# Optimization experiments

Measured on AMD Instinct MI355X. Metric: run time of the kernel, lower is better.

Reference implementation:

```python
import jax, jax.numpy as jnp
import numpy as np

EMBED_DIM = 1024
HEADS = 16
HEAD_DIM = EMBED_DIM // HEADS


def setup_inputs() -> dict:
    key = jax.random.key(0)
    ks = jax.random.split(key, 9)
    D = EMBED_DIM
    s = 1.0 / np.sqrt(D)
    x = jax.random.normal(ks[0], (4, 2048, D), dtype=jnp.float32)
    Wq = jax.random.uniform(ks[1], (D, D), jnp.float32, -s, s)
    bq = jnp.zeros((D,), jnp.float32)
    Wk = jax.random.uniform(ks[2], (D, D), jnp.float32, -s, s)
    bk = jnp.zeros((D,), jnp.float32)
    Wv = jax.random.uniform(ks[3], (D, D), jnp.float32, -s, s)
    bv = jnp.zeros((D,), jnp.float32)
    Wo = jax.random.uniform(ks[4], (D, D), jnp.float32, -s, s)
    bo = jnp.zeros((D,), jnp.float32)
    gamma = jnp.ones((D,), jnp.float32)
    beta = jnp.zeros((D,), jnp.float32)
    return {"x": x, "Wq": Wq, "bq": bq, "Wk": Wk, "bk": bk,
            "Wv": Wv, "bv": bv, "Wo": Wo, "bo": bo,
            "gamma": gamma, "beta": beta}


def reference(x, Wq, bq, Wk, bk, Wv, bv, Wo, bo, gamma, beta):
    B, S, D = x.shape
    H, Dh = HEADS, HEAD_DIM
    # projections -> [B, H, S, Dh]
    q = (x @ Wq + bq).reshape(B, S, H, Dh).transpose(0, 2, 1, 3)
    k = (x @ Wk + bk).reshape(B, S, H, Dh).transpose(0, 2, 1, 3)
    v = (x @ Wv + bv).reshape(B, S, H, Dh).transpose(0, 2, 1, 3)
    scores = jnp.einsum('bhqd,bhkd->bhqk', q, k) / jnp.sqrt(jnp.float32(Dh))
    attn = jax.nn.softmax(scores, axis=-1)  # dropout is identity in eval
    ctx = jnp.einsum('bhqk,bhkd->bhqd', attn, v)
    ctx = ctx.transpose(0, 2, 1, 3).reshape(B, S, D)
    out = ctx @ Wo + bo
    # residual + LayerNorm (eps=1e-5, torch default)
    h = out + x
    mu = jnp.mean(h, axis=-1, keepdims=True)
    var = jnp.mean(jnp.square(h - mu), axis=-1, keepdims=True)
    return (h - mu) * jax.lax.rsqrt(var + 1e-5) * gamma + beta
```

## Files before the change

kernel.cpp:

```cpp
#include <hip/hip_runtime.h>
#include <hip/hip_bf16.h>
#include <stdint.h>

typedef short sh4 __attribute__((ext_vector_type(4)));
typedef short sh8 __attribute__((ext_vector_type(8)));
typedef float fl4 __attribute__((ext_vector_type(4)));
typedef float f32x4 __attribute__((ext_vector_type(4)));
typedef float f32x16 __attribute__((ext_vector_type(16)));
typedef uint32_t u32x4 __attribute__((ext_vector_type(4)));

static __device__ __forceinline__ short f2bf(float f) {
  union { float f; uint32_t u; } v;
  v.f = f;
  uint32_t r = v.u + 0x7fffu + ((v.u >> 16) & 1u);
  return (short)(r >> 16);
}

static __device__ __forceinline__ uint32_t cvt_pk_bf16(float a, float b) {
  uint32_t r;
  asm("v_cvt_pk_bf16_f32 %0, %1, %2" : "=v"(r) : "v"(a), "v"(b));
  return r;
}

static __device__ __forceinline__ void pl32swap(uint32_t& a, uint32_t& b) {
  asm volatile("v_permlane32_swap_b32 %0, %1" : "+v"(a), "+v"(b));
}

static __device__ __forceinline__ void gload_lds16(const void* g, void* l) {
  __builtin_amdgcn_global_load_lds((const __attribute__((address_space(1))) void*)g,
                                   (__attribute__((address_space(3))) void*)l, 16, 0, 0);
}

__global__ __launch_bounds__(256) void k_wt(const float* __restrict__ Wq, const float* __restrict__ Wk,
                                            const float* __restrict__ Wv, const float* __restrict__ Wo,
                                            short* __restrict__ Tq, short* __restrict__ Tk,
                                            short* __restrict__ Tv, short* __restrict__ To) {
  const float* W = blockIdx.z == 0 ? Wq : blockIdx.z == 1 ? Wk : blockIdx.z == 2 ? Wv : Wo;
  short* T = blockIdx.z == 0 ? Tq : blockIdx.z == 1 ? Tk : blockIdx.z == 2 ? Tv : To;
  __shared__ float tile[32][33];
  int n0 = blockIdx.x * 32, k0 = blockIdx.y * 32;
  int tx = threadIdx.x, ty = threadIdx.y;
#pragma unroll
  for (int p = 0; p < 4; p++) tile[ty + 8 * p][tx] = W[(size_t)(k0 + ty + 8 * p) * 1024 + n0 + tx];
  __syncthreads();
#pragma unroll
  for (int p = 0; p < 4; p++) T[(size_t)(n0 + ty + 8 * p) * 1024 + k0 + tx] = f2bf(tile[tx][ty + 8 * p]);
}

__global__ __launch_bounds__(256) void k_cvtx(const float* __restrict__ x, short* __restrict__ o) {
  int i = blockIdx.x * 256 + threadIdx.x;
  fl4 v = ((const fl4*)x)[i];
  sh4 r;
#pragma unroll
  for (int j = 0; j < 4; j++) r[j] = f2bf(v[j]);
  ((sh4*)o)[i] = r;
}

#define GEMM_PIPE_LOOP(STAGE_BODY, COMPUTE_BODY)                         \
  STAGE_BODY(0, 0);                                                      \
  STAGE_BODY(1, 1);                                                      \
  {                                                                      \
    int bufc = 0, bufs = 2;                                              \
    for (int it = 0; it < 32; it++) {                                    \
      if (it < 31)                                                       \
        asm volatile("s_waitcnt vmcnt(4)" ::: "memory");                 \
      else                                                               \
        asm volatile("s_waitcnt vmcnt(0)" ::: "memory");                 \
      __builtin_amdgcn_s_barrier();                                      \
      if (it + 2 < 32) { STAGE_BODY(it + 2, bufs); }                     \
      __builtin_amdgcn_sched_barrier(0);                                 \
      { int buf = bufc; COMPUTE_BODY }                                   \
      bufc = bufc == 2 ? 0 : bufc + 1;                                   \
      bufs = bufs == 2 ? 0 : bufs + 1;                                   \
      asm volatile("" ::: "memory");                                     \
    }                                                                    \
  }

__global__ __launch_bounds__(256) void k_qk(const short* __restrict__ A, const short* __restrict__ WT2,
                                            const float* __restrict__ bq, const float* __restrict__ bk,
                                            short* __restrict__ Qo, short* __restrict__ Ko, float qscale) {
  __shared__ __align__(16) short As[3][128 * 32];
  __shared__ __align__(16) short Bs[3][128 * 32];
  const int xcd = blockIdx.x & 7, j = blockIdx.x >> 3;
  const int m0 = (xcd + 8 * (j & 7)) * 128, n0 = (j >> 3) * 128;
  const int sec = n0 >> 10;
  const float* bias = sec == 0 ? bq : bk;
  short* Out = sec == 0 ? Qo : Ko;
  const float scale = sec == 0 ? qscale : 1.f;
  const int t = threadIdx.x;
  const int lane = t & 63, w = t >> 6;
  const int wr = w >> 1, wc = w & 1;
  const int l15 = lane & 15, g = lane >> 4;
  f32x4 acc[4][4];
#pragma unroll
  for (int mi = 0; mi < 4; mi++)
#pragma unroll
    for (int ni = 0; ni < 4; ni++) acc[mi][ni] = (f32x4){0.f, 0.f, 0.f, 0.f};

#define QK_STAGE(kt, buf)                                                                     \
  {                                                                                           \
    int r0 = w * 32;                                                                          \
    _Pragma("unroll") for (int i = 0; i < 2; i++) {                                           \
      int row = r0 + i * 16 + (lane >> 2);                                                    \
      gload_lds16(&A[(size_t)(m0 + row) * 1024 + (kt) * 32 + (lane & 3) * 8],                 \
                  &As[buf][(r0 + i * 16) * 32]);                                              \
      gload_lds16(&WT2[(size_t)(n0 + row) * 1024 + (kt) * 32 + (lane & 3) * 8],               \
                  &Bs[buf][(r0 + i * 16) * 32]);                                              \
    }                                                                                         \
  }

#define QK_COMPUTE                                                                            \
  sh8 a[4], b[4];                                                                             \
  _Pragma("unroll") for (int i = 0; i < 4; i++)                                               \
      a[i] = *(sh8*)&As[buf][(wr * 64 + i * 16 + l15) * 32 + g * 8];                          \
  _Pragma("unroll") for (int i = 0; i < 4; i++)                                               \
      b[i] = *(sh8*)&Bs[buf][(wc * 64 + i * 16 + l15) * 32 + g * 8];                          \
  _Pragma("unroll") for (int mi = 0; mi < 4; mi++)                                            \
      _Pragma("unroll") for (int ni = 0; ni < 4; ni++)                                        \
          acc[mi][ni] = __builtin_amdgcn_mfma_f32_16x16x32_bf16(b[ni], a[mi], acc[mi][ni], 0, 0, 0);

  GEMM_PIPE_LOOP(QK_STAGE, QK_COMPUTE)

#pragma unroll
  for (int ni = 0; ni < 4; ni++) {
    int nbase = n0 + wc * 64 + ni * 16 + g * 4;
    int nn0 = nbase & 1023;
    fl4 bv4 = *(const fl4*)&bias[nn0];
    int h = nn0 >> 6, dh0 = nn0 & 63;
#pragma unroll
    for (int mi = 0; mi < 4; mi++) {
      int m = m0 + wr * 64 + mi * 16 + l15;
      int bb = m >> 11, s = m & 2047;
      uint2 dd;
      dd.x = cvt_pk_bf16((acc[mi][ni][0] + bv4[0]) * scale, (acc[mi][ni][1] + bv4[1]) * scale);
      dd.y = cvt_pk_bf16((acc[mi][ni][2] + bv4[2]) * scale, (acc[mi][ni][3] + bv4[3]) * scale);
      *(uint2*)&Out[(((size_t)bb * 16 + h) * 2048 + s) * 64 + dh0] = dd;
    }
  }
}

__global__ __launch_bounds__(256) void k_v(const short* __restrict__ A, const short* __restrict__ WTv,
                                           const float* __restrict__ bv, short* __restrict__ Vo) {
  __shared__ __align__(16) short As[3][128 * 32];
  __shared__ __align__(16) short Bs[3][128 * 32];
  const int xcd = blockIdx.x & 7, j = blockIdx.x >> 3;
  const int m0 = (xcd + 8 * (j & 7)) * 128, n0 = (j >> 3) * 128;
  const int t = threadIdx.x;
  const int lane = t & 63, w = t >> 6;
  const int wr = w >> 1, wc = w & 1;
  const int l15 = lane & 15, g = lane >> 4;
  f32x4 acc[4][4];
#pragma unroll
  for (int mi = 0; mi < 4; mi++)
#pragma unroll
    for (int ni = 0; ni < 4; ni++) acc[mi][ni] = (f32x4){0.f, 0.f, 0.f, 0.f};

#define V_STAGE(kt, buf)                                                                      \
  {                                                                                           \
    int r0 = w * 32;                                                                          \
    _Pragma("unroll") for (int i = 0; i < 2; i++) {                                           \
      int row = r0 + i * 16 + (lane >> 2);                                                    \
      gload_lds16(&A[(size_t)(m0 + row) * 1024 + (kt) * 32 + (lane & 3) * 8],                 \
                  &As[buf][(r0 + i * 16) * 32]);                                              \
      gload_lds16(&WTv[(size_t)(n0 + row) * 1024 + (kt) * 32 + (lane & 3) * 8],               \
                  &Bs[buf][(r0 + i * 16) * 32]);                                              \
    }                                                                                         \
  }

#define V_COMPUTE                                                                             \
  sh8 a[4], b[4];                                                                             \
  _Pragma("unroll") for (int i = 0; i < 4; i++)                                               \
      a[i] = *(sh8*)&As[buf][(wr * 64 + i * 16 + l15) * 32 + g * 8];                          \
  _Pragma("unroll") for (int i = 0; i < 4; i++)                                               \
      b[i] = *(sh8*)&Bs[buf][(wc * 64 + i * 16 + l15) * 32 + g * 8];                          \
  _Pragma("unroll") for (int mi = 0; mi < 4; mi++)                                            \
      _Pragma("unroll") for (int ni = 0; ni < 4; ni++)                                        \
          acc[mi][ni] = __builtin_amdgcn_mfma_f32_16x16x32_bf16(a[mi], b[ni], acc[mi][ni], 0, 0, 0);

  GEMM_PIPE_LOOP(V_STAGE, V_COMPUTE)

#pragma unroll
  for (int ni = 0; ni < 4; ni++) {
    int col = n0 + wc * 64 + ni * 16 + l15;
    int nn = col & 1023;
    float bvv = bv[nn];
    int h = nn >> 6, dh = nn & 63;
#pragma unroll
    for (int mi = 0; mi < 4; mi++) {
      int mr = m0 + wr * 64 + mi * 16 + g * 4;
      int bb = mr >> 11, s = mr & 2047;
      uint2 dd;
      dd.x = cvt_pk_bf16(acc[mi][ni][0] + bvv, acc[mi][ni][1] + bvv);
      dd.y = cvt_pk_bf16(acc[mi][ni][2] + bvv, acc[mi][ni][3] + bvv);
      *(uint2*)&Vo[(((size_t)bb * 16 + h) * 64 + dh) * 2048 + s] = dd;
    }
  }
}

__global__ __launch_bounds__(256) void k_oproj(const short* __restrict__ A, const short* __restrict__ BT,
                                               const float* __restrict__ bias, const float* __restrict__ X,
                                               float* __restrict__ Out) {
  __shared__ __align__(16) short As[3][128 * 32];
  __shared__ __align__(16) short Bs[3][128 * 32];
  const int xcd = blockIdx.x & 7, j = blockIdx.x >> 3;
  const int m0 = (xcd + 8 * (j & 7)) * 128, n0 = (j >> 3) * 128;
  const int t = threadIdx.x;
  const int lane = t & 63, w = t >> 6;
  const int wr = w >> 1, wc = w & 1;
  const int l15 = lane & 15, g = lane >> 4;
  f32x4 acc[4][4];
#pragma unroll
  for (int mi = 0; mi < 4; mi++)
#pragma unroll
    for (int ni = 0; ni < 4; ni++) acc[mi][ni] = (f32x4){0.f, 0.f, 0.f, 0.f};

#define O_STAGE(kt, buf)                                                                      \
  {                                                                                           \
    int r0 = w * 32;                                                                          \
    _Pragma("unroll") for (int i = 0; i < 2; i++) {                                           \
      int row = r0 + i * 16 + (lane >> 2);                                                    \
      gload_lds16(&A[(size_t)(m0 + row) * 1024 + (kt) * 32 + (lane & 3) * 8],                 \
                  &As[buf][(r0 + i * 16) * 32]);                                              \
      gload_lds16(&BT[(size_t)(n0 + row) * 1024 + (kt) * 32 + (lane & 3) * 8],                \
                  &Bs[buf][(r0 + i * 16) * 32]);                                              \
    }                                                                                         \
  }

#define O_COMPUTE                                                                             \
  sh8 a[4], b[4];                                                                             \
  _Pragma("unroll") for (int i = 0; i < 4; i++)                                               \
      a[i] = *(sh8*)&As[buf][(wr * 64 + i * 16 + l15) * 32 + g * 8];                          \
  _Pragma("unroll") for (int i = 0; i < 4; i++)                                               \
      b[i] = *(sh8*)&Bs[buf][(wc * 64 + i * 16 + l15) * 32 + g * 8];                          \
  _Pragma("unroll") for (int mi = 0; mi < 4; mi++)                                            \
      _Pragma("unroll") for (int ni = 0; ni < 4; ni++)                                        \
          acc[mi][ni] = __builtin_amdgcn_mfma_f32_16x16x32_bf16(b[ni], a[mi], acc[mi][ni], 0, 0, 0);

  GEMM_PIPE_LOOP(O_STAGE, O_COMPUTE)

#pragma unroll
  for (int ni = 0; ni < 4; ni++) {
    int nbase = n0 + wc * 64 + ni * 16 + g * 4;
    fl4 bv4 = *(const fl4*)&bias[nbase];
#pragma unroll
    for (int mi = 0; mi < 4; mi++) {
      int m = m0 + wr * 64 + mi * 16 + l15;
      fl4 xv = *(const fl4*)&X[(size_t)m * 1024 + nbase];
      fl4 r;
#pragma unroll
      for (int e = 0; e < 4; e++) r[e] = acc[mi][ni][e] + bv4[e] + xv[e];
      *(fl4*)&Out[(size_t)m * 1024 + nbase] = r;
    }
  }
}

__global__ __launch_bounds__(512, 4) void k_attn(const short* __restrict__ Q, const short* __restrict__ K,
                                                 const short* __restrict__ Vt, short* __restrict__ CTX) {
  const int nid = (blockIdx.x & 7) * 64 + (blockIdx.x >> 3);
  const int qbi = nid & 7, h = (nid >> 3) & 15, b = nid >> 7;
  const int q0 = qbi * 256;
  const size_t ho = (((size_t)b * 16 + h) * 2048) * 64;
  const short* Qh = Q + ho;
  const short* Kh = K + ho;
  const short* Vh = Vt + ho;
  __shared__ __align__(16) short Ks[3][8 * 512];
  __shared__ __align__(16) short Vs[3][8 * 512];
  const int t = threadIdx.x, lane = t & 63, w = t >> 6;
  const int l31 = lane & 31, hi = lane >> 5;

  sh8 qreg[4];
#pragma unroll
  for (int ks = 0; ks < 4; ks++)
    qreg[ks] = *(const sh8*)&Qh[(size_t)(q0 + w * 32 + l31) * 64 + ks * 16 + hi * 8];

  f32x16 oc0, oc1;
#pragma unroll
  for (int r = 0; r < 16; r++) { oc0[r] = 0.f; oc1[r] = 0.f; }
  float l_s = 0.f;

  auto stage = [&](int kt, int buf) {
    gload_lds16(&Kh[(size_t)(kt * 64 + (w >> 2) * 32 + l31) * 64 + (w & 3) * 16 + hi * 8],
                (char*)&Ks[buf][0] + w * 1024);
    gload_lds16(&Vh[(size_t)((w >> 2) * 32 + l31) * 2048 + kt * 64 + (w & 3) * 16 + hi * 8],
                (char*)&Vs[buf][0] + w * 1024);
  };

  stage(0, 0);
  stage(1, 1);
  int bufc = 0, bufs = 2;

  for (int kt = 0; kt < 32; kt++) {
    if (kt < 31)
      asm volatile("s_waitcnt vmcnt(2)" ::: "memory");
    else
      asm volatile("s_waitcnt vmcnt(0)" ::: "memory");
    __builtin_amdgcn_s_barrier();
    if (kt + 2 < 32) stage(kt + 2, bufs);
    __builtin_amdgcn_sched_barrier(0);

    f32x16 s0, s1;
#pragma unroll
    for (int r = 0; r < 16; r++) { s0[r] = 0.f; s1[r] = 0.f; }
    __builtin_amdgcn_s_setprio(1);
#pragma unroll
    for (int ks = 0; ks < 4; ks++) {
      sh8 ak0 = *(sh8*)((char*)&Ks[bufc][0] + ks * 1024 + lane * 16);
      sh8 ak1 = *(sh8*)((char*)&Ks[bufc][0] + (4 + ks) * 1024 + lane * 16);
      s0 = __builtin_amdgcn_mfma_f32_32x32x16_bf16(ak0, qreg[ks], s0, 0, 0, 0);
      s1 = __builtin_amdgcn_mfma_f32_32x32x16_bf16(ak1, qreg[ks], s1, 0, 0, 0);
    }
    __builtin_amdgcn_s_setprio(0);

    float ps = 0.f;
#pragma unroll
    for (int r = 0; r < 16; r++) { s0[r] = __builtin_amdgcn_exp2f(s0[r]); ps += s0[r]; }
#pragma unroll
    for (int r = 0; r < 16; r++) { s1[r] = __builtin_amdgcn_exp2f(s1[r]); ps += s1[r]; }
    l_s += ps;

    u32x4 pw0, pw1, pw2, pw3;
    {
      uint32_t a0 = cvt_pk_bf16(s0[0], s0[1]), a1 = cvt_pk_bf16(s0[2], s0[3]);
      uint32_t b0 = cvt_pk_bf16(s0[4], s0[5]), b1 = cvt_pk_bf16(s0[6], s0[7]);
      uint32_t c0 = cvt_pk_bf16(s0[8], s0[9]), c1 = cvt_pk_bf16(s0[10], s0[11]);
      uint32_t d0 = cvt_pk_bf16(s0[12], s0[13]), d1 = cvt_pk_bf16(s0[14], s0[15]);
      pl32swap(a0, b0); pl32swap(a1, b1); pl32swap(c0, d0); pl32swap(c1, d1);
      pw0 = (u32x4){a0, a1, b0, b1};
      pw1 = (u32x4){c0, c1, d0, d1};
      a0 = cvt_pk_bf16(s1[0], s1[1]); a1 = cvt_pk_bf16(s1[2], s1[3]);
      b0 = cvt_pk_bf16(s1[4], s1[5]); b1 = cvt_pk_bf16(s1[6], s1[7]);
      c0 = cvt_pk_bf16(s1[8], s1[9]); c1 = cvt_pk_bf16(s1[10], s1[11]);
      d0 = cvt_pk_bf16(s1[12], s1[13]); d1 = cvt_pk_bf16(s1[14], s1[15]);
      pl32swap(a0, b0); pl32swap(a1, b1); pl32swap(c0, d0); pl32swap(c1, d1);
      pw2 = (u32x4){a0, a1, b0, b1};
      pw3 = (u32x4){c0, c1, d0, d1};
    }
    sh8 pb0 = __builtin_bit_cast(sh8, pw0), pb1 = __builtin_bit_cast(sh8, pw1);
    sh8 pb2 = __builtin_bit_cast(sh8, pw2), pb3 = __builtin_bit_cast(sh8, pw3);

    __builtin_amdgcn_s_setprio(1);
#pragma unroll
    for (int ks = 0; ks < 4; ks++) {
      sh8 pb = ks == 0 ? pb0 : ks == 1 ? pb1 : ks == 2 ? pb2 : pb3;
      sh8 av0 = *(sh8*)((char*)&Vs[bufc][0] + ks * 1024 + lane * 16);
      sh8 av1 = *(sh8*)((char*)&Vs[bufc][0] + (4 + ks) * 1024 + lane * 16);
      oc0 = __builtin_amdgcn_mfma_f32_32x32x16_bf16(av0, pb, oc0, 0, 0, 0);
      oc1 = __builtin_amdgcn_mfma_f32_32x32x16_bf16(av1, pb, oc1, 0, 0, 0);
    }
    __builtin_amdgcn_s_setprio(0);
    bufc = bufc == 2 ? 0 : bufc + 1;
    bufs = bufs == 2 ? 0 : bufs + 1;
    asm volatile("" ::: "memory");
  }

  l_s += __shfl_xor(l_s, 32);
  float li = 1.f / l_s;
  int s = q0 + w * 32 + l31;
  size_t obase = (((size_t)b * 2048 + s) * 16 + h) * 64;
#pragma unroll
  for (int rq = 0; rq < 4; rq++) {
    uint2 dd;
    dd.x = cvt_pk_bf16(oc0[4 * rq] * li, oc0[4 * rq + 1] * li);
    dd.y = cvt_pk_bf16(oc0[4 * rq + 2] * li, oc0[4 * rq + 3] * li);
    *(uint2*)&CTX[obase + rq * 8 + hi * 4] = dd;
    dd.x = cvt_pk_bf16(oc1[4 * rq] * li, oc1[4 * rq + 1] * li);
    dd.y = cvt_pk_bf16(oc1[4 * rq + 2] * li, oc1[4 * rq + 3] * li);
    *(uint2*)&CTX[obase + 32 + rq * 8 + hi * 4] = dd;
  }
}

__global__ __launch_bounds__(256) void k_ln(float* __restrict__ Out, const float* __restrict__ gamma,
                                            const float* __restrict__ beta) {
  int row = blockIdx.x * 4 + (threadIdx.x >> 6);
  int lane = threadIdx.x & 63;
  float* p = Out + (size_t)row * 1024;
  fl4 v[4];
  float s = 0.f, s2 = 0.f;
#pragma unroll
  for (int j = 0; j < 4; j++) {
    v[j] = *(fl4*)&p[lane * 4 + j * 256];
#pragma unroll
    for (int e = 0; e < 4; e++) { s += v[j][e]; s2 += v[j][e] * v[j][e]; }
  }
#pragma unroll
  for (int off = 1; off < 64; off <<= 1) {
    s += __shfl_xor(s, off);
    s2 += __shfl_xor(s2, off);
  }
  float mu = s * (1.f / 1024.f);
  float var = s2 * (1.f / 1024.f) - mu * mu;
  float inv = rsqrtf(var + 1e-5f);
#pragma unroll
  for (int j = 0; j < 4; j++) {
    fl4 r;
#pragma unroll
    for (int e = 0; e < 4; e++) {
      int c = lane * 4 + j * 256 + e;
      r[e] = (v[j][e] - mu) * inv * gamma[c] + beta[c];
    }
    *(fl4*)&p[lane * 4 + j * 256] = r;
  }
}

extern "C" void kernel_launch(void* const* d_in, const int* in_sizes, int n_in,
                              void* d_out, int out_size, void* d_ws, size_t ws_size,
                              hipStream_t stream) {
  (void)in_sizes; (void)n_in; (void)out_size; (void)ws_size;
  const float* x = (const float*)d_in[0];
  const float* Wq = (const float*)d_in[1];
  const float* bq = (const float*)d_in[2];
  const float* Wk = (const float*)d_in[3];
  const float* bk = (const float*)d_in[4];
  const float* Wv = (const float*)d_in[5];
  const float* bv = (const float*)d_in[6];
  const float* Wo = (const float*)d_in[7];
  const float* bo = (const float*)d_in[8];
  const float* gamma = (const float*)d_in[9];
  const float* beta = (const float*)d_in[10];
  float* out = (float*)d_out;
  char* ws = (char*)d_ws;
  short* xbf = (short*)(ws);
  short* wtq = (short*)(ws + (16ull << 20));
  short* wtk = (short*)(ws + (18ull << 20));
  short* wtv = (short*)(ws + (20ull << 20));
  short* wto = (short*)(ws + (22ull << 20));
  short* qb  = (short*)(ws + (24ull << 20));
  short* kbuf = (short*)(ws + (40ull << 20));
  short* vbuf = (short*)(ws + (56ull << 20));
  short* ctx = (short*)(ws + (72ull << 20));

  const float QSCALE = 0.125f * 1.44269504088896f;

  k_wt<<<dim3(32, 32, 4), dim3(32, 8), 0, stream>>>(Wq, Wk, Wv, Wo, wtq, wtk, wtv, wto);
  k_cvtx<<<8192, 256, 0, stream>>>(x, xbf);
  k_qk<<<1024, 256, 0, stream>>>(xbf, wtq, bq, bk, qb, kbuf, QSCALE);
  k_v<<<512, 256, 0, stream>>>(xbf, wtv, bv, vbuf);
  k_attn<<<512, 512, 0, stream>>>(qb, kbuf, vbuf, ctx);
  k_oproj<<<512, 256, 0, stream>>>(ctx, wto, bo, x, out);
  k_ln<<<2048, 256, 0, stream>>>(out, gamma, beta);
}
```

Baseline: 213.9 us.

## Software-pipeline attention loop: overlap PV of previous tile with QK of current

Restructures the attention inner loop so the P·V MFMAs for tile kt-1 are issued right after the Q·K MFMAs for tile kt, letting exp/convert work overlap with matrix ops. The packed probabilities are carried across iterations in registers and a drain step follows the loop. V gets a fourth LDS buffer so the previous tile's V stays valid while the next ones are prefetched. This costs extra LDS and more live registers, which could lower occupancy under the launch bounds.

```diff
diff --git a/kernel.cpp b/kernel.cpp
--- a/kernel.cpp
+++ b/kernel.cpp
@@ -264,7 +264,7 @@
   const short* Kh = K + ho;
   const short* Vh = Vt + ho;
   __shared__ __align__(16) short Ks[3][8 * 512];
-  __shared__ __align__(16) short Vs[3][8 * 512];
+  __shared__ __align__(16) short Vs[4][8 * 512];
   const int t = threadIdx.x, lane = t & 63, w = t >> 6;
   const int l31 = lane & 31, hi = lane >> 5;
 
@@ -273,21 +273,25 @@
   for (int ks = 0; ks < 4; ks++)
     qreg[ks] = *(const sh8*)&Qh[(size_t)(q0 + w * 32 + l31) * 64 + ks * 16 + hi * 8];
 
-  f32x16 oc0, oc1;
-#pragma unroll
-  for (int r = 0; r < 16; r++) { oc0[r] = 0.f; oc1[r] = 0.f; }
+  f32x16 zinit;
+#pragma unroll
+  for (int r = 0; r < 16; r++) zinit[r] = 0.f;
+
+  f32x16 oc0 = zinit, oc1 = zinit;
   float l_s = 0.f;
-
-  auto stage = [&](int kt, int buf) {
+  u32x4 pwp[4];
+
+  auto stageK = [&](int kt, int buf) {
     gload_lds16(&Kh[(size_t)(kt * 64 + (w >> 2) * 32 + l31) * 64 + (w & 3) * 16 + hi * 8],
                 (char*)&Ks[buf][0] + w * 1024);
+  };
+  auto stageV = [&](int kt, int buf) {
     gload_lds16(&Vh[(size_t)((w >> 2) * 32 + l31) * 2048 + kt * 64 + (w & 3) * 16 + hi * 8],
                 (char*)&Vs[buf][0] + w * 1024);
   };
 
-  stage(0, 0);
-  stage(1, 1);
-  int bufc = 0, bufs = 2;
+  stageK(0, 0); stageV(0, 0);
+  stageK(1, 1); stageV(1, 1);
 
   for (int kt = 0; kt < 32; kt++) {
     if (kt < 31)
@@ -295,19 +299,35 @@
     else
       asm volatile("s_waitcnt vmcnt(0)" ::: "memory");
     __builtin_amdgcn_s_barrier();
-    if (kt + 2 < 32) stage(kt + 2, bufs);
+    if (kt + 2 < 32) { stageK(kt + 2, (kt + 2) % 3); stageV(kt + 2, (kt + 2) & 3); }
     __builtin_amdgcn_sched_barrier(0);
+    const int kbuf = kt % 3;
 
     f32x16 s0, s1;
-#pragma unroll
-    for (int r = 0; r < 16; r++) { s0[r] = 0.f; s1[r] = 0.f; }
     __builtin_amdgcn_s_setprio(1);
 #pragma unroll
     for (int ks = 0; ks < 4; ks++) {
-      sh8 ak0 = *(sh8*)((char*)&Ks[bufc][0] + ks * 1024 + lane * 16);
-      sh8 ak1 = *(sh8*)((char*)&Ks[bufc][0] + (4 + ks) * 1024 + lane * 16);
-      s0 = __builtin_amdgcn_mfma_f32_32x32x16_bf16(ak0, qreg[ks], s0, 0, 0, 0);
-      s1 = __builtin_amdgcn_mfma_f32_32x32x16_bf16(ak1, qreg[ks], s1, 0, 0, 0);
+      sh8 ak0 = *(sh8*)((char*)&Ks[kbuf][0] + ks * 1024 + lane * 16);
+      sh8 ak1 = *(sh8*)((char*)&Ks[kbuf][0] + (4 + ks) * 1024 + lane * 16);
+      if (ks == 0) {
+        s0 = __builtin_amdgcn_mfma_f32_32x32x16_bf16(ak0, qreg[0], zinit, 0, 0, 0);
+        s1 = __builtin_amdgcn_mfma_f32_32x32x16_bf16(ak1, qreg[0], zinit, 0, 0, 0);
+      } else {
+        s0 = __builtin_amdgcn_mfma_f32_32x32x16_bf16(ak0, qreg[ks], s0, 0, 0, 0);
+        s1 = __builtin_amdgcn_mfma_f32_32x32x16_bf16(ak1, qreg[ks], s1, 0, 0, 0);
+      }
+    }
+
+    if (kt > 0) {
+      const int vb = (kt - 1) & 3;
+#pragma unroll
+      for (int ks = 0; ks < 4; ks++) {
+        sh8 pb = __builtin_bit_cast(sh8, pwp[ks]);
+        sh8 av0 = *(sh8*)((char*)&Vs[vb][0] + ks * 1024 + lane * 16);
+        sh8 av1 = *(sh8*)((char*)&Vs[vb][0] + (4 + ks) * 1024 + lane * 16);
+        oc0 = __builtin_amdgcn_mfma_f32_32x32x16_bf16(av0, pb, oc0, 0, 0, 0);
+        oc1 = __builtin_amdgcn_mfma_f32_32x32x16_bf16(av1, pb, oc1, 0, 0, 0);
+      }
     }
     __builtin_amdgcn_s_setprio(0);
 
@@ -318,39 +338,37 @@
     for (int r = 0; r < 16; r++) { s1[r] = __builtin_amdgcn_exp2f(s1[r]); ps += s1[r]; }
     l_s += ps;
 
-    u32x4 pw0, pw1, pw2, pw3;
     {
       uint32_t a0 = cvt_pk_bf16(s0[0], s0[1]), a1 = cvt_pk_bf16(s0[2], s0[3]);
       uint32_t b0 = cvt_pk_bf16(s0[4], s0[5]), b1 = cvt_pk_bf16(s0[6], s0[7]);
       uint32_t c0 = cvt_pk_bf16(s0[8], s0[9]), c1 = cvt_pk_bf16(s0[10], s0[11]);
       uint32_t d0 = cvt_pk_bf16(s0[12], s0[13]), d1 = cvt_pk_bf16(s0[14], s0[15]);
       pl32swap(a0, b0); pl32swap(a1, b1); pl32swap(c0, d0); pl32swap(c1, d1);
-      pw0 = (u32x4){a0, a1, b0, b1};
-      pw1 = (u32x4){c0, c1, d0, d1};
+      pwp[0] = (u32x4){a0, a1, b0, b1};
+      pwp[1] = (u32x4){c0, c1, d0, d1};
       a0 = cvt_pk_bf16(s1[0], s1[1]); a1 = cvt_pk_bf16(s1[2], s1[3]);
       b0 = cvt_pk_bf16(s1[4], s1[5]); b1 = cvt_pk_bf16(s1[6], s1[7]);
       c0 = cvt_pk_bf16(s1[8], s1[9]); c1 = cvt_pk_bf16(s1[10], s1[11]);
       d0 = cvt_pk_bf16(s1[12], s1[13]); d1 = cvt_pk_bf16(s1[14], s1[15]);
       pl32swap(a0, b0); pl32swap(a1, b1); pl32swap(c0, d0); pl32swap(c1, d1);
-      pw2 = (u32x4){a0, a1, b0, b1};
-      pw3 = (u32x4){c0, c1, d0, d1};
-    }
-    sh8 pb0 = __builtin_bit_cast(sh8, pw0), pb1 = __builtin_bit_cast(sh8, pw1);
-    sh8 pb2 = __builtin_bit_cast(sh8, pw2), pb3 = __builtin_bit_cast(sh8, pw3);
-
+      pwp[2] = (u32x4){a0, a1, b0, b1};
+      pwp[3] = (u32x4){c0, c1, d0, d1};
+    }
+    asm volatile("" ::: "memory");
+  }
+
+  {
+    const int vb = 31 & 3;
     __builtin_amdgcn_s_setprio(1);
 #pragma unroll
     for (int ks = 0; ks < 4; ks++) {
-      sh8 pb = ks == 0 ? pb0 : ks == 1 ? pb1 : ks == 2 ? pb2 : pb3;
-      sh8 av0 = *(sh8*)((char*)&Vs[bufc][0] + ks * 1024 + lane * 16);
-      sh8 av1 = *(sh8*)((char*)&Vs[bufc][0] + (4 + ks) * 1024 + lane * 16);
+      sh8 pb = __builtin_bit_cast(sh8, pwp[ks]);
+      sh8 av0 = *(sh8*)((char*)&Vs[vb][0] + ks * 1024 + lane * 16);
+      sh8 av1 = *(sh8*)((char*)&Vs[vb][0] + (4 + ks) * 1024 + lane * 16);
       oc0 = __builtin_amdgcn_mfma_f32_32x32x16_bf16(av0, pb, oc0, 0, 0, 0);
       oc1 = __builtin_amdgcn_mfma_f32_32x32x16_bf16(av1, pb, oc1, 0, 0, 0);
     }
     __builtin_amdgcn_s_setprio(0);
-    bufc = bufc == 2 ? 0 : bufc + 1;
-    bufs = bufs == 2 ? 0 : bufs + 1;
-    asm volatile("" ::: "memory");
   }
 
   l_s += __shfl_xor(l_s, 32);
```

New measurement: 212.9 us. Within noise of the previous version (-0.5%).
